# Kernel tuning notes

Measured on AMD Instinct MI355X. Metric: run time of the kernel, lower is better.

The kernel has to match this reference:

```python
import jax, jax.numpy as jnp
import numpy as np
from jax import lax

N_WIRES = 4
EPS_BN = 1e-5

def _conv(x, w, b):
    y = lax.conv_general_dilated(x, w, (1, 1), 'SAME',
                                 dimension_numbers=('NCHW', 'OIHW', 'NCHW'))
    return y + b[None, :, None, None]

def _bn2d(x, g, b):
    mu = jnp.mean(x, axis=(0, 2, 3), keepdims=True)
    var = jnp.var(x, axis=(0, 2, 3), keepdims=True)
    return (x - mu) * lax.rsqrt(var + EPS_BN) * g[None, :, None, None] + b[None, :, None, None]

def _maxpool2(x):
    return lax.reduce_window(x, -jnp.inf, lax.max, (1, 1, 2, 2), (1, 1, 2, 2), 'VALID')

def _ry(t):
    c, s = jnp.cos(t / 2), jnp.sin(t / 2)
    return jnp.stack([jnp.stack([c, -s], -1), jnp.stack([s, c], -1)], -2).astype(jnp.complex64)

def _rz(t):
    tc = t.astype(jnp.complex64)
    em, ep = jnp.exp(-0.5j * tc), jnp.exp(0.5j * tc)
    z = jnp.zeros_like(em)
    return jnp.stack([jnpp_stack := jnp.stack([em, z], -1), jnp.stack([z, ep], -1)], -2)

def _rx(t):
    c = jnp.cos(t / 2).astype(jnp.complex64)
    s = (-1j) * jnp.sin(t / 2).astype(jnp.complex64)
    return jnp.stack([jnp.stack([c, s], -1), jnp.stack([s, c], -1)], -2)

def _apply_1q(state, U, q):
    # state: (B,2,2,2,2); U: (2,2) shared or (B,2,2) per-sample
    a = jnp.moveaxis(state, 1 + q, 1)
    if U.ndim == 2:
        a = jnp.einsum('ij,bj...->bi...', U, a)
    else:
        a = jnp.einsum('bij,bj...->bi...', U, a)
    return jnp.moveaxis(a, 1, 1 + q)

def _cnot(state, c, t):
    a = jnp.moveaxis(state, (1 + c, 1 + t), (1, 2))
    a = jnp.stack([a[:, 0], jnp.flip(a[:, 1], axis=1)], axis=1)
    return jnp.moveaxis(a, (1, 2), (1 + c, 1 + t))

def _circuit(scaled, theta, rho):
    # scaled: (B, 4) angles; theta, rho: (4, 3)
    B = scaled.shape[0]
    state = jnp.zeros((B,) + (2,) * N_WIRES, jnp.complex64)
    state = state.at[(slice(None),) + (0,) * N_WIRES].set(1.0 + 0j)
    for i in range(N_WIRES):
        state = _apply_1q(state, _ry(scaled[:, i]), i)
    for i in range(N_WIRES):
        state = _apply_1q(state, _ry(theta[i, 0]), i)
        state = _apply_1q(state, _rz(theta[i, 1]), i)
        state = _apply_1q(state, _rx(theta[i, 2]), i)
    for i in range(N_WIRES - 1):
        state = _cnot(state, i, i + 1)
    for i in range(N_WIRES):
        state = _apply_1q(state, _ry(rho[i, 0]), i)
        state = _apply_1q(state, _rz(rho[i, 1]), i)
        state = _apply_1q(state, _rx(rho[i, 2]), i)
    for i in range(N_WIRES - 1):
        state = _cnot(state, i + 1, i)
    probs = jnp.abs(state) ** 2  # (B,2,2,2,2)
    exps = []
    for i in range(N_WIRES):
        p = jnp.moveaxis(probs, 1 + i, 1)
        exps.append(jnp.sum(p[:, 0], axis=(1, 2, 3)) - jnp.sum(p[:, 1], axis=(1, 2, 3)))
    return jnp.stack(exps, axis=1)  # (B,4)

def setup_inputs() -> dict:
    key = jax.random.key(0)
    ks = jax.random.split(key, 8)
    B = 128
    return {
        'x': jax.random.normal(ks[0], (B, 1, 224, 224), jnp.float32),
        'conv1_w': jax.random.normal(ks[1], (8, 1, 3, 3), jnp.float32) * 0.1,
        'conv1_b': jnp.zeros((8,), jnp.float32),
        'bn1_g': jnp.ones((8,), jnp.float32),
        'bn1_b': jnp.zeros((8,), jnp.float32),
        'conv2_w': jax.random.normal(ks[2], (16, 8, 3, 3), jnp.float32) * 0.1,
        'conv2_b': jnp.zeros((16,), jnp.float32),
        'bn2_g': jnp.ones((16,), jnp.float32),
        'bn2_b': jnp.zeros((16,), jnp.float32),
        'theta': jax.random.normal(ks[3], (4, 3), jnp.float32),
        'rho': jax.random.normal(ks[4], (4, 3), jnp.float32),
        'norm_g': jnp.ones((4,), jnp.float32),
        'norm_b': jnp.zeros((4,), jnp.float32),
    }

def reference(x, conv1_w, conv1_b, bn1_g, bn1_b, conv2_w, conv2_b, bn2_g, bn2_b,
              theta, rho, norm_g, norm_b):
    h = jax.nn.relu(_bn2d(_conv(x, conv1_w, conv1_b), bn1_g, bn1_b))
    h = _maxpool2(h)
    h = jax.nn.relu(_bn2d(_conv(h, conv2_w, conv2_b), bn2_g, bn2_b))
    h = _maxpool2(h)
    feat = jnp.mean(h, axis=(2, 3))          # AdaptiveAvgPool2d((1,1)) + flatten -> (B,16)
    feat = feat[:, :N_WIRES]                  # (B,4)
    scaled = (feat - jnp.mean(feat)) / (jnp.std(feat, ddof=1) + 1e-6) * jnp.pi
    out = _circuit(scaled, theta, rho)        # (B,4) real
    mu = jnp.mean(out, axis=0, keepdims=True)
    var = jnp.var(out, axis=0, keepdims=True)
    return (out - mu) * lax.rsqrt(var + EPS_BN) * norm_g[None, :] + norm_b[None, :]
```

## Files before the change

### kernel.cpp

```cpp
#include <hip/hip_runtime.h>
#include <math.h>

#define H1 224
#define W1 224
#define H2 112
#define W2 112
#define HP 56
#define WP 56

#define NS 32
#define SLOT_STRIDE 64

struct C2 { float re, im; };
__device__ __forceinline__ C2 cmul(C2 a, C2 b) {
    return C2{fmaf(a.re, b.re, -a.im * b.im), fmaf(a.re, b.im, a.im * b.re)};
}
__device__ __forceinline__ C2 cadd(C2 a, C2 b) { return C2{a.re + b.re, a.im + b.im}; }

template <int S>
__device__ __forceinline__ void ap1s(C2* st, C2 u00, C2 u01, C2 u10, C2 u11) {
#pragma unroll
    for (int i = 0; i < 16; i++) {
        if (i & S) continue;
        C2 a0 = st[i], a1 = st[i + S];
        st[i]     = cadd(cmul(u00, a0), cmul(u01, a1));
        st[i + S] = cadd(cmul(u10, a0), cmul(u11, a1));
    }
}
template <int SC, int STT>
__device__ __forceinline__ void cnot_s(C2* st) {
#pragma unroll
    for (int i = 0; i < 16; i++)
        if ((i & SC) && !(i & STT)) { C2 t = st[i]; st[i] = st[i + STT]; st[i + STT] = t; }
}
struct M2 { C2 m[2][2]; };
__device__ __forceinline__ M2 mmul(const M2& A, const M2& B) {
    M2 R;
#pragma unroll
    for (int i = 0; i < 2; i++)
#pragma unroll
        for (int j = 0; j < 2; j++)
            R.m[i][j] = cadd(cmul(A.m[i][0], B.m[0][j]), cmul(A.m[i][1], B.m[1][j]));
    return R;
}
__device__ __forceinline__ M2 combined_u(const float* __restrict__ p) {
    float c0 = cosf(0.5f * p[0]), s0 = sinf(0.5f * p[0]);
    float c1 = cosf(0.5f * p[1]), s1 = sinf(0.5f * p[1]);
    float c2 = cosf(0.5f * p[2]), s2 = sinf(0.5f * p[2]);
    M2 Ry = {{{{c0, 0.f}, {-s0, 0.f}}, {{s0, 0.f}, {c0, 0.f}}}};
    M2 Rz = {{{{c1, -s1}, {0.f, 0.f}}, {{0.f, 0.f}, {c1, s1}}}};
    M2 Rx = {{{{c2, 0.f}, {0.f, -s2}}, {{0.f, -s2}, {c2, 0.f}}}};
    return mmul(Rx, mmul(Rz, Ry));
}

template <int Q>
__device__ __forceinline__ void rows_reduce(float* red, const float* vals, int tid) {
#pragma unroll
    for (int q = 0; q < Q; q++) red[q * 256 + tid] = vals[q];
    __syncthreads();
#pragma unroll
    for (int s = 128; s > 0; s >>= 1) {
        for (int idx = tid; idx < Q * s; idx += 256) {
            int row = idx / s, i = idx - row * s;
            red[row * 256 + i] += red[row * 256 + i + s];
        }
        __syncthreads();
    }
}

__global__ void zero_ws(float* ws, int n) {
    int i = blockIdx.x * blockDim.x + threadIdx.x;
    if (i < n) ws[i] = 0.f;
}

__device__ __forceinline__ float slot_sum(const float* stats, int c) {
    float s = 0.f;
#pragma unroll
    for (int sl = 0; sl < NS; sl++) s += stats[sl * SLOT_STRIDE + c];
    return s;
}

__global__ void conv1_pool_stats(const float* __restrict__ x, const float* __restrict__ w,
                                 const float* __restrict__ bias, const float* __restrict__ g1,
                                 float* __restrict__ stats, float* __restrict__ p1ext) {
    __shared__ float red[16 * 256];
    int strip = blockIdx.x;
    int b = blockIdx.y;
    int tid = threadIdx.x;
    const float* xb = x + (size_t)b * H1 * W1;
    float sums[8], sqs[8], pm[8], ext8[8];
    bool gp[8];
#pragma unroll
    for (int c = 0; c < 8; c++) { sums[c] = 0.f; sqs[c] = 0.f; gp[c] = g1[c] >= 0.f; }
    int col = tid;
    if (col < W1) {
        bool cl = col > 0, cr = col < W1 - 1;
        int row0 = strip * 8;
        float a0, a1, a2, b0, b1, b2, c0, c1, c2;
        {
            int r = row0 - 1;
            if (r >= 0) {
                a0 = cl ? xb[r * W1 + col - 1] : 0.f;
                a1 = xb[r * W1 + col];
                a2 = cr ? xb[r * W1 + col + 1] : 0.f;
            } else { a0 = a1 = a2 = 0.f; }
            r = row0;
            b0 = cl ? xb[r * W1 + col - 1] : 0.f;
            b1 = xb[r * W1 + col];
            b2 = cr ? xb[r * W1 + col + 1] : 0.f;
        }
        for (int rr = 0; rr < 8; rr++) {
            int rn = row0 + rr + 1;
            if (rn < H1) {
                c0 = cl ? xb[rn * W1 + col - 1] : 0.f;
                c1 = xb[rn * W1 + col];
                c2 = cr ? xb[rn * W1 + col + 1] : 0.f;
            } else { c0 = c1 = c2 = 0.f; }
#pragma unroll
            for (int c = 0; c < 8; c++) {
                float acc = bias[c];
                acc = fmaf(w[c * 9 + 0], a0, acc);
                acc = fmaf(w[c * 9 + 1], a1, acc);
                acc = fmaf(w[c * 9 + 2], a2, acc);
                acc = fmaf(w[c * 9 + 3], b0, acc);
                acc = fmaf(w[c * 9 + 4], b1, acc);
                acc = fmaf(w[c * 9 + 5], b2, acc);
                acc = fmaf(w[c * 9 + 6], c0, acc);
                acc = fmaf(w[c * 9 + 7], c1, acc);
                acc = fmaf(w[c * 9 + 8], c2, acc);
                sums[c] += acc;
                sqs[c] = fmaf(acc, acc, sqs[c]);
                if ((rr & 1) == 0) {
                    pm[c] = acc;
                } else {
                    float m = gp[c] ? fmaxf(pm[c], acc) : fminf(pm[c], acc);
                    float mo = __shfl_xor(m, 1, 64);
                    ext8[c] = gp[c] ? fmaxf(m, mo) : fminf(m, mo);
                }
            }
            if ((rr & 1) == 1 && (col & 1) == 0) {
                int prow = strip * 4 + (rr >> 1);
                int pcol = col >> 1;
                float* dst = p1ext + ((((size_t)b * H2 + prow) * W2 + pcol) << 3);
                ((float4*)dst)[0] = make_float4(ext8[0], ext8[1], ext8[2], ext8[3]);
                ((float4*)dst)[1] = make_float4(ext8[4], ext8[5], ext8[6], ext8[7]);
            }
            a0 = b0; a1 = b1; a2 = b2;
            b0 = c0; b1 = c1; b2 = c2;
        }
    }
    float vals[16];
#pragma unroll
    for (int c = 0; c < 8; c++) { vals[c] = sums[c]; vals[8 + c] = sqs[c]; }
    rows_reduce<16>(red, vals, tid);
    int slot = (b * 28 + strip) & (NS - 1);
    if (tid < 16) atomicAdd(stats + slot * SLOT_STRIDE + tid, red[tid * 256]);
}

__global__ void conv1_stats(const float* __restrict__ x, const float* __restrict__ w,
                            const float* __restrict__ bias, float* __restrict__ stats) {
    __shared__ float red[16 * 256];
    int strip = blockIdx.x;
    int b = blockIdx.y;
    int tid = threadIdx.x;
    const float* xb = x + (size_t)b * H1 * W1;
    float sums[8], sqs[8];
#pragma unroll
    for (int c = 0; c < 8; c++) { sums[c] = 0.f; sqs[c] = 0.f; }
    int col = tid;
    if (col < W1) {
        bool cl = col > 0, cr = col < W1 - 1;
        int row0 = strip * 8;
        float a0, a1, a2, b0, b1, b2, c0, c1, c2;
        {
            int r = row0 - 1;
            if (r >= 0) {
                a0 = cl ? xb[r * W1 + col - 1] : 0.f;
                a1 = xb[r * W1 + col];
                a2 = cr ? xb[r * W1 + col + 1] : 0.f;
            } else { a0 = a1 = a2 = 0.f; }
            r = row0;
            b0 = cl ? xb[r * W1 + col - 1] : 0.f;
            b1 = xb[r * W1 + col];
            b2 = cr ? xb[r * W1 + col + 1] : 0.f;
        }
        for (int rr = 0; rr < 8; rr++) {
            int rn = row0 + rr + 1;
            if (rn < H1) {
                c0 = cl ? xb[rn * W1 + col - 1] : 0.f;
                c1 = xb[rn * W1 + col];
                c2 = cr ? xb[rn * W1 + col + 1] : 0.f;
            } else { c0 = c1 = c2 = 0.f; }
#pragma unroll
            for (int c = 0; c < 8; c++) {
                float acc = bias[c];
                acc = fmaf(w[c * 9 + 0], a0, acc);
                acc = fmaf(w[c * 9 + 1], a1, acc);
                acc = fmaf(w[c * 9 + 2], a2, acc);
                acc = fmaf(w[c * 9 + 3], b0, acc);
                acc = fmaf(w[c * 9 + 4], b1, acc);
                acc = fmaf(w[c * 9 + 5], b2, acc);
                acc = fmaf(w[c * 9 + 6], c0, acc);
                acc = fmaf(w[c * 9 + 7], c1, acc);
                acc = fmaf(w[c * 9 + 8], c2, acc);
                sums[c] += acc;
                sqs[c] = fmaf(acc, acc, sqs[c]);
            }
            a0 = b0; a1 = b1; a2 = b2;
            b0 = c0; b1 = c1; b2 = c2;
        }
    }
    float vals[16];
#pragma unroll
    for (int c = 0; c < 8; c++) { vals[c] = sums[c]; vals[8 + c] = sqs[c]; }
    rows_reduce<16>(red, vals, tid);
    int slot = (b * 28 + strip) & (NS - 1);
    if (tid < 16) atomicAdd(stats + slot * SLOT_STRIDE + tid, red[tid * 256]);
}

template <int PH, int PW>
__device__ __forceinline__ void build_h1_tile(const float* __restrict__ xb,
                                              float (*h1t)[PH][PW],
                                              const float* __restrict__ w1,
                                              const float* __restrict__ b1,
                                              const float* sc1, const float* sh1,
                                              int oy0, int ox0, int tid) {
    for (int i = tid; i < PH * PW; i += 256) {
        int p = i / PW, q = i % PW;
        int hy = oy0 + p, hx = ox0 + q;
        bool ok = (hy >= 0 && hy < H2 && hx >= 0 && hx < W2);
        float xp[5][5];
        if (hy >= 1 && hy <= H2 - 2 && hx >= 1 && hx <= W2 - 2) {
            const float* bp = xb + (2 * hy - 1) * W1 + (2 * hx - 1);
#pragma unroll
            for (int r = 0; r < 5; r++)
#pragma unroll
                for (int c = 0; c < 5; c++) xp[r][c] = bp[r * W1 + c];
        } else if (ok) {
#pragma unroll
            for (int r = 0; r < 5; r++)
#pragma unroll
                for (int c = 0; c < 5; c++) {
                    int gy = 2 * hy - 1 + r, gx = 2 * hx - 1 + c;
                    xp[r][c] = (gy >= 0 && gy < H1 && gx >= 0 && gx < W1) ? xb[gy * W1 + gx] : 0.f;
                }
        }
#pragma unroll
        for (int c = 0; c < 8; c++) {
            float mx = 0.f;
            if (ok) {
                mx = -INFINITY;
#pragma unroll
                for (int dy = 0; dy < 2; dy++)
#pragma unroll
                    for (int dx = 0; dx < 2; dx++) {
                        float acc = b1[c];
#pragma unroll
                        for (int ky = 0; ky < 3; ky++)
#pragma unroll
                            for (int kx = 0; kx < 3; kx++)
                                acc = fmaf(w1[c * 9 + ky * 3 + kx], xp[dy + ky][dx + kx], acc);
                        mx = fmaxf(mx, fmaxf(fmaf(acc, sc1[c], sh1[c]), 0.f));
                    }
            }
            h1t[c][p][q] = mx;
        }
    }
}

__global__ __launch_bounds__(256, 4) void conv2_stats_slim(
        const float* __restrict__ p1ext, const float* __restrict__ g1,
        const float* __restrict__ be1, const float* __restrict__ stats1,
        const float* __restrict__ w2, const float* __restrict__ b2,
        const float* __restrict__ g2,
        float* __restrict__ stats2, float* __restrict__ p2ext, float N1) {
    __shared__ __align__(16) float h1t[8][34][34];
    __shared__ float sc1[8], sh1[8];
    int b = blockIdx.z;
    int Y0 = blockIdx.y * 32, X0 = blockIdx.x * 32;
    int ty = threadIdx.y, tx = threadIdx.x;
    int tid = ty * 16 + tx;
    if (tid < 8) {
        float su = slot_sum(stats1, tid), sq = slot_sum(stats1, 8 + tid);
        float mu = su / N1;
        float var = sq / N1 - mu * mu;
        float sc = g1[tid] * rsqrtf(var + 1e-5f);
        sc1[tid] = sc;
        sh1[tid] = be1[tid] - mu * sc;
    }
    __syncthreads();
    const float* pb = p1ext + (((size_t)b * H2) * W2 << 3);
    for (int i = tid; i < 34 * 34; i += 256) {
        int p = i / 34, q = i % 34;
        int hy = Y0 - 1 + p, hx = X0 - 1 + q;
        if (hy >= 0 && hy < H2 && hx >= 0 && hx < W2) {
            const float* cp = pb + (((size_t)hy * W2 + hx) << 3);
            float4 u = ((const float4*)cp)[0];
            float4 v = ((const float4*)cp)[1];
            h1t[0][p][q] = fmaxf(fmaf(u.x, sc1[0], sh1[0]), 0.f);
            h1t[1][p][q] = fmaxf(fmaf(u.y, sc1[1], sh1[1]), 0.f);
            h1t[2][p][q] = fmaxf(fmaf(u.z, sc1[2], sh1[2]), 0.f);
            h1t[3][p][q] = fmaxf(fmaf(u.w, sc1[3], sh1[3]), 0.f);
            h1t[4][p][q] = fmaxf(fmaf(v.x, sc1[4], sh1[4]), 0.f);
            h1t[5][p][q] = fmaxf(fmaf(v.y, sc1[5], sh1[5]), 0.f);
            h1t[6][p][q] = fmaxf(fmaf(v.z, sc1[6], sh1[6]), 0.f);
            h1t[7][p][q] = fmaxf(fmaf(v.w, sc1[7], sh1[7]), 0.f);
        } else {
#pragma unroll
            for (int c = 0; c < 8; c++) h1t[c][p][q] = 0.f;
        }
    }
    __syncthreads();
    float acc[4][2][2];
#pragma unroll
    for (int co = 0; co < 4; co++)
#pragma unroll
        for (int dy = 0; dy < 2; dy++)
#pragma unroll
            for (int dx = 0; dx < 2; dx++) acc[co][dy][dx] = b2[co];
#pragma unroll
    for (int ci = 0; ci < 8; ci++) {
        float win[4][4];
#pragma unroll
        for (int r = 0; r < 4; r++) {
            const float2* rp = (const float2*)&h1t[ci][2 * ty + r][2 * tx];
            float2 u = rp[0], v = rp[1];
            win[r][0] = u.x; win[r][1] = u.y; win[r][2] = v.x; win[r][3] = v.y;
        }
#pragma unroll
        for (int co = 0; co < 4; co++)
#pragma unroll
            for (int ky = 0; ky < 3; ky++)
#pragma unroll
                for (int kx = 0; kx < 3; kx++) {
                    float wv = w2[co * 72 + ci * 9 + ky * 3 + kx];
#pragma unroll
                    for (int dy = 0; dy < 2; dy++)
#pragma unroll
                        for (int dx = 0; dx < 2; dx++)
                            acc[co][dy][dx] = fmaf(wv, win[dy + ky][dx + kx], acc[co][dy][dx]);
                }
    }
    int cy0 = Y0 + 2 * ty, cx0 = X0 + 2 * tx;
    bool vy0 = cy0 < H2, vy1 = cy0 + 1 < H2, vx0 = cx0 < W2, vx1 = cx0 + 1 < W2;
    float vals[8];
#pragma unroll
    for (int co = 0; co < 4; co++) {
        float s = 0.f, q = 0.f;
        if (vy0 && vx0) { float a = acc[co][0][0]; s += a; q = fmaf(a, a, q); }
        if (vy0 && vx1) { float a = acc[co][0][1]; s += a; q = fmaf(a, a, q); }
        if (vy1 && vx0) { float a = acc[co][1][0]; s += a; q = fmaf(a, a, q); }
        if (vy1 && vx1) { float a = acc[co][1][1]; s += a; q = fmaf(a, a, q); }
        vals[co] = s;
        vals[4 + co] = q;
    }
    {
        int hy = (Y0 >> 1) + ty, hx = (X0 >> 1) + tx;
        if (hy < HP && hx < WP) {
#pragma unroll
            for (int co = 0; co < 4; co++) {
                float mx = fmaxf(fmaxf(acc[co][0][0], acc[co][0][1]),
                                 fmaxf(acc[co][1][0], acc[co][1][1]));
                float mn = fminf(fminf(acc[co][0][0], acc[co][0][1]),
                                 fminf(acc[co][1][0], acc[co][1][1]));
                p2ext[(((size_t)b * 4 + co) * HP + hy) * WP + hx] = (g2[co] >= 0.f) ? mx : mn;
            }
        }
    }
    __syncthreads();
    float* red = (float*)h1t;
    rows_reduce<8>(red, vals, tid);
    int slot = ((b * 16) + blockIdx.y * 4 + blockIdx.x) & (NS - 1);
    if (tid < 8) atomicAdd(stats2 + slot * SLOT_STRIDE + tid, red[tid * 256]);
}

template <bool STORE>
__global__ __launch_bounds__(256, 4) void conv2_stats_fused(
        const float* __restrict__ x, const float* __restrict__ w1,
        const float* __restrict__ b1, const float* __restrict__ g1,
        const float* __restrict__ be1, const float* __restrict__ stats1,
        const float* __restrict__ w2, const float* __restrict__ b2,
        float* __restrict__ stats2,
        float* __restrict__ pmax, float* __restrict__ pmin, float N1) {
    __shared__ __align__(16) float h1t[8][34][34];
    __shared__ float sc1[8], sh1[8];
    int b = blockIdx.z;
    int Y0 = blockIdx.y * 32, X0 = blockIdx.x * 32;
    int ty = threadIdx.y, tx = threadIdx.x;
    int tid = ty * 16 + tx;
    if (tid < 8) {
        float su = slot_sum(stats1, tid), sq = slot_sum(stats1, 8 + tid);
        float mu = su / N1;
        float var = sq / N1 - mu * mu;
        float sc = g1[tid] * rsqrtf(var + 1e-5f);
        sc1[tid] = sc;
        sh1[tid] = be1[tid] - mu * sc;
    }
    __syncthreads();
    const float* xb = x + (size_t)b * H1 * W1;
    build_h1_tile<34, 34>(xb, h1t, w1, b1, sc1, sh1, Y0 - 1, X0 - 1, tid);
    __syncthreads();
    float acc[4][2][2];
#pragma unroll
    for (int co = 0; co < 4; co++)
#pragma unroll
        for (int dy = 0; dy < 2; dy++)
#pragma unroll
            for (int dx = 0; dx < 2; dx++) acc[co][dy][dx] = b2[co];
#pragma unroll
    for (int ci = 0; ci < 8; ci++) {
        float win[4][4];
#pragma unroll
        for (int r = 0; r < 4; r++) {
            const float2* rp = (const float2*)&h1t[ci][2 * ty + r][2 * tx];
            float2 u = rp[0], v = rp[1];
            win[r][0] = u.x; win[r][1] = u.y; win[r][2] = v.x; win[r][3] = v.y;
        }
#pragma unroll
        for (int co = 0; co < 4; co++)
#pragma unroll
            for (int ky = 0; ky < 3; ky++)
#pragma unroll
                for (int kx = 0; kx < 3; kx++) {
                    float wv = w2[co * 72 + ci * 9 + ky * 3 + kx];
#pragma unroll
                    for (int dy = 0; dy < 2; dy++)
#pragma unroll
                        for (int dx = 0; dx < 2; dx++)
                            acc[co][dy][dx] = fmaf(wv, win[dy + ky][dx + kx], acc[co][dy][dx]);
                }
    }
    int cy0 = Y0 + 2 * ty, cx0 = X0 + 2 * tx;
    bool vy0 = cy0 < H2, vy1 = cy0 + 1 < H2, vx0 = cx0 < W2, vx1 = cx0 + 1 < W2;
    float vals[8];
#pragma unroll
    for (int co = 0; co < 4; co++) {
        float s = 0.f, q = 0.f;
        if (vy0 && vx0) { float a = acc[co][0][0]; s += a; q = fmaf(a, a, q); }
        if (vy0 && vx1) { float a = acc[co][0][1]; s += a; q = fmaf(a, a, q); }
        if (vy1 && vx0) { float a = acc[co][1][0]; s += a; q = fmaf(a, a, q); }
        if (vy1 && vx1) { float a = acc[co][1][1]; s += a; q = fmaf(a, a, q); }
        vals[co] = s;
        vals[4 + co] = q;
    }
    if (STORE) {
        int hy = (Y0 >> 1) + ty, hx = (X0 >> 1) + tx;
        if (hy < HP && hx < WP) {
#pragma unroll
            for (int co = 0; co < 4; co++) {
                float mx = fmaxf(fmaxf(acc[co][0][0], acc[co][0][1]),
                                 fmaxf(acc[co][1][0], acc[co][1][1]));
                float mn = fminf(fminf(acc[co][0][0], acc[co][0][1]),
                                 fminf(acc[co][1][0], acc[co][1][1]));
                size_t idx = (((size_t)b * 4 + co) * HP + hy) * WP + hx;
                pmax[idx] = mx;
                pmin[idx] = mn;
            }
        }
    }
    __syncthreads();
    float* red = (float*)h1t;
    rows_reduce<8>(red, vals, tid);
    int slot = ((b * 16) + blockIdx.y * 4 + blockIdx.x) & (NS - 1);
    if (tid < 8) atomicAdd(stats2 + slot * SLOT_STRIDE + tid, red[tid * 256]);
}

__global__ void pool_bn_mean(const float* __restrict__ pmax, const float* __restrict__ pmin,
                             const float* __restrict__ g2, const float* __restrict__ be2,
                             const float* __restrict__ stats2,
                             float* __restrict__ featbuf, float N2) {
    __shared__ float red[256];
    int co = blockIdx.x & 3;
    int b = blockIdx.x >> 2;
    int tid = threadIdx.x;
    float su = slot_sum(stats2, co), sq = slot_sum(stats2, 4 + co);
    float mu = su / N2;
    float var = sq / N2 - mu * mu;
    float sc = g2[co] * rsqrtf(var + 1e-5f);
    float sh = be2[co] - mu * sc;
    const float* P = (sc >= 0.f ? pmax : pmin) + ((size_t)b * 4 + co) * (HP * WP);
    float s = 0.f;
    for (int i = tid; i < HP * WP; i += 256) s += fmaxf(fmaf(P[i], sc, sh), 0.f);
    red[tid] = s;
    __syncthreads();
    for (int st = 128; st > 0; st >>= 1) {
        if (tid < st) red[tid] += red[tid + st];
        __syncthreads();
    }
    if (tid == 0) featbuf[(size_t)b * 4 + co] = red[0];
}

__global__ void conv2_final_fused(const float* __restrict__ x, const float* __restrict__ w1,
                                  const float* __restrict__ b1, const float* __restrict__ g1,
                                  const float* __restrict__ be1,
                                  const float* __restrict__ stats1,
                                  const float* __restrict__ w2, const float* __restrict__ b2,
                                  const float* __restrict__ g2, const float* __restrict__ be2,
                                  const float* __restrict__ stats2,
                                  float* __restrict__ featbuf, float N1, float N2) {
    __shared__ __align__(16) float h1t[8][34][34];
    __shared__ float sc1[8], sh1[8];
    __shared__ float sc2[4], sh2[4];
    int b = blockIdx.z;
    int py0 = blockIdx.y * 16, px0 = blockIdx.x * 16;
    int ty = threadIdx.y, tx = threadIdx.x;
    int tid = ty * 16 + tx;
    if (tid < 8) {
        float su = slot_sum(stats1, tid), sq = slot_sum(stats1, 8 + tid);
        float mu = su / N1;
        float var = sq / N1 - mu * mu;
        float sc = g1[tid] * rsqrtf(var + 1e-5f);
        sc1[tid] = sc;
        sh1[tid] = be1[tid] - mu * sc;
    }
    if (tid >= 16 && tid < 20) {
        int j = tid - 16;
        float su = slot_sum(stats2, j), sq = slot_sum(stats2, 4 + j);
        float mu = su / N2;
        float var = sq / N2 - mu * mu;
        float sc = g2[j] * rsqrtf(var + 1e-5f);
        sc2[j] = sc;
        sh2[j] = be2[j] - mu * sc;
    }
    __syncthreads();
    const float* xb = x + (size_t)b * H1 * W1;
    build_h1_tile<34, 34>(xb, h1t, w1, b1, sc1, sh1, 2 * py0 - 1, 2 * px0 - 1, tid);
    __syncthreads();
    bool valid = (py0 + ty < HP) && (px0 + tx < WP);
    float acc[4][2][2];
#pragma unroll
    for (int co = 0; co < 4; co++)
#pragma unroll
        for (int dy = 0; dy < 2; dy++)
#pragma unroll
            for (int dx = 0; dx < 2; dx++) acc[co][dy][dx] = b2[co];
#pragma unroll
    for (int ci = 0; ci < 8; ci++) {
        float win[4][4];
#pragma unroll
        for (int r = 0; r < 4; r++) {
            const float2* rp = (const float2*)&h1t[ci][2 * ty + r][2 * tx];
            float2 u = rp[0], v = rp[1];
            win[r][0] = u.x; win[r][1] = u.y; win[r][2] = v.x; win[r][3] = v.y;
        }
#pragma unroll
        for (int co = 0; co < 4; co++)
#pragma unroll
            for (int ky = 0; ky < 3; ky++)
#pragma unroll
                for (int kx = 0; kx < 3; kx++) {
                    float wv = w2[co * 72 + ci * 9 + ky * 3 + kx];
#pragma unroll
                    for (int dy = 0; dy < 2; dy++)
#pragma unroll
                        for (int dx = 0; dx < 2; dx++)
                            acc[co][dy][dx] = fmaf(wv, win[dy + ky][dx + kx], acc[co][dy][dx]);
                }
    }
    float vals[4];
#pragma unroll
    for (int co = 0; co < 4; co++) {
        float mx = -INFINITY;
#pragma unroll
        for (int dy = 0; dy < 2; dy++)
#pragma unroll
            for (int dx = 0; dx < 2; dx++)
                mx = fmaxf(mx, fmaxf(fmaf(acc[co][dy][dx], sc2[co], sh2[co]), 0.f));
        vals[co] = valid ? mx : 0.f;
    }
    __syncthreads();
    float* red = (float*)h1t;
    rows_reduce<4>(red, vals, tid);
    if (tid < 4) atomicAdd(featbuf + (size_t)b * 4 + tid, red[tid * 256]);
}

__device__ __forceinline__ float bsum(float v, float* lds) {
#pragma unroll
    for (int off = 32; off; off >>= 1) v += __shfl_xor(v, off, 64);
    __syncthreads();
    if ((threadIdx.x & 63) == 0) lds[threadIdx.x >> 6] = v;
    __syncthreads();
    float r = 0.f;
    int nw = (int)(blockDim.x + 63) >> 6;
#pragma clang loop unroll(disable)
    for (int i = 0; i < nw; i++) r += lds[i];
    return r;
}

__global__ void finalize(const float* __restrict__ featbuf, const float* __restrict__ theta,
                         const float* __restrict__ rho, const float* __restrict__ ng,
                         const float* __restrict__ nb, float* __restrict__ out, int B) {
    __shared__ float lds[16];
    int b = threadIdx.x;
    float f[4];
#pragma unroll
    for (int j = 0; j < 4; j++) f[j] = featbuf[b * 4 + j] * (1.f / (HP * WP));
    float n = 4.f * (float)B;
    float mean = bsum(f[0] + f[1] + f[2] + f[3], lds) / n;
    float d2 = 0.f;
#pragma unroll
    for (int j = 0; j < 4; j++) { float d = f[j] - mean; d2 += d * d; }
    float var1 = bsum(d2, lds) / (n - 1.f);
    float stdv = sqrtf(fmaxf(var1, 0.f)) + 1e-6f;
    const float PI = 3.14159265358979323846f;
    float cs[4], sn[4];
#pragma unroll
    for (int j = 0; j < 4; j++) {
        float sc = (f[j] - mean) / stdv * PI;
        cs[j] = cosf(0.5f * sc);
        sn[j] = sinf(0.5f * sc);
    }
    C2 st[16];
    {
        float amp[16];
        amp[1] = sn[3]; amp[0] = cs[3];
#pragma unroll
        for (int k = 0; k < 2; k++) { amp[k + 2] = amp[k] * sn[2]; amp[k] *= cs[2]; }
#pragma unroll
        for (int k = 0; k < 4; k++) { amp[k + 4] = amp[k] * sn[1]; amp[k] *= cs[1]; }
#pragma unroll
        for (int k = 0; k < 8; k++) { amp[k + 8] = amp[k] * sn[0]; amp[k] *= cs[0]; }
#pragma unroll
        for (int i = 0; i < 16; i++) st[i] = C2{amp[i], 0.f};
    }
#pragma clang loop unroll(disable)
    for (int l = 0; l < 2; l++) {
        const float* p = (l == 0) ? theta : rho;
#pragma clang loop unroll(disable)
        for (int i = 0; i < 4; i++) {
            M2 U = combined_u(p + i * 3);
            switch (i) {
            case 0: ap1s<8>(st, U.m[0][0], U.m[0][1], U.m[1][0], U.m[1][1]); break;
            case 1: ap1s<4>(st, U.m[0][0], U.m[0][1], U.m[1][0], U.m[1][1]); break;
            case 2: ap1s<2>(st, U.m[0][0], U.m[0][1], U.m[1][0], U.m[1][1]); break;
            default: ap1s<1>(st, U.m[0][0], U.m[0][1], U.m[1][0], U.m[1][1]); break;
            }
        }
        if (l == 0) { cnot_s<8, 4>(st); cnot_s<4, 2>(st); cnot_s<2, 1>(st); }
        else        { cnot_s<4, 8>(st); cnot_s<2, 4>(st); cnot_s<1, 2>(st); }
    }
    float e[4];
#pragma unroll
    for (int qb = 0; qb < 4; qb++) {
        int m = 8 >> qb;
        float p0 = 0.f, p1 = 0.f;
#pragma unroll
        for (int i = 0; i < 16; i++) {
            float pr = st[i].re * st[i].re + st[i].im * st[i].im;
            if (i & m) p1 += pr; else p0 += pr;
        }
        e[qb] = p0 - p1;
    }
#pragma clang loop unroll(disable)
    for (int j = 0; j < 4; j++) {
        float mu = bsum(e[j], lds) / (float)B;
        float dv = e[j] - mu;
        float v = bsum(dv * dv, lds) / (float)B;
        out[b * 4 + j] = fmaf(dv, rsqrtf(v + 1e-5f) * ng[j], nb[j]);
    }
}

extern "C" void kernel_launch(void* const* d_in, const int* in_sizes, int n_in,
                              void* d_out, int out_size, void* d_ws, size_t ws_size,
                              hipStream_t stream) {
    const float* x     = (const float*)d_in[0];
    const float* w1    = (const float*)d_in[1];
    const float* b1    = (const float*)d_in[2];
    const float* g1    = (const float*)d_in[3];
    const float* be1   = (const float*)d_in[4];
    const float* w2    = (const float*)d_in[5];
    const float* b2    = (const float*)d_in[6];
    const float* g2    = (const float*)d_in[7];
    const float* be2   = (const float*)d_in[8];
    const float* theta = (const float*)d_in[9];
    const float* rho   = (const float*)d_in[10];
    const float* ng    = (const float*)d_in[11];
    const float* nb    = (const float*)d_in[12];
    float* out = (float*)d_out;

    int B = in_sizes[0] / (H1 * W1);

    float* ws = (float*)d_ws;
    float* stats1 = ws;
    float* stats2 = ws + NS * SLOT_STRIDE;
    float* featbuf = ws + 2 * NS * SLOT_STRIDE;
    float* bufs = featbuf + (size_t)B * 4;

    size_t common = (size_t)(2 * NS * SLOT_STRIDE) + (size_t)B * 4;
    size_t p2n = (size_t)B * 4 * HP * WP;
    size_t p1n = (size_t)B * 8 * H2 * W2;
    size_t needA = (common + p2n + p1n) * sizeof(float);
    size_t needB = (common + 2 * p2n) * sizeof(float);
    bool tierA = ws_size >= needA;
    bool tierB = !tierA && ws_size >= needB;

    float N1 = (float)B * H1 * W1;
    float N2 = (float)B * H2 * W2;
    int nz = (int)common;

    zero_ws<<<(nz + 255) / 256, 256, 0, stream>>>(ws, nz);
    if (tierA) {
        float* p2ext = bufs;
        float* p1ext = bufs + p2n;
        conv1_pool_stats<<<dim3(28, B), 256, 0, stream>>>(x, w1, b1, g1, stats1, p1ext);
        conv2_stats_slim<<<dim3(4, 4, B), dim3(16, 16), 0, stream>>>(
            p1ext, g1, be1, stats1, w2, b2, g2, stats2, p2ext, N1);
        pool_bn_mean<<<B * 4, 256, 0, stream>>>(p2ext, p2ext, g2, be2, stats2, featbuf, N2);
        finalize<<<1, B, 0, stream>>>(featbuf, theta, rho, ng, nb, out, B);
    } else if (tierB) {
        float* pmax = bufs;
        float* pmin = bufs + p2n;
        conv1_stats<<<dim3(28, B), 256, 0, stream>>>(x, w1, b1, stats1);
        conv2_stats_fused<true><<<dim3(4, 4, B), dim3(16, 16), 0, stream>>>(
            x, w1, b1, g1, be1, stats1, w2, b2, stats2, pmax, pmin, N1);
        pool_bn_mean<<<B * 4, 256, 0, stream>>>(pmax, pmin, g2, be2, stats2, featbuf, N2);
        finalize<<<1, B, 0, stream>>>(featbuf, theta, rho, ng, nb, out, B);
    } else {
        conv1_stats<<<dim3(28, B), 256, 0, stream>>>(x, w1, b1, stats1);
        conv2_stats_fused<false><<<dim3(4, 4, B), dim3(16, 16), 0, stream>>>(
            x, w1, b1, g1, be1, stats1, w2, b2, stats2, nullptr, nullptr, N1);
        conv2_final_fused<<<dim3(4, 4, B), dim3(16, 16), 0, stream>>>(
            x, w1, b1, g1, be1, stats1, w2, b2, g2, be2, stats2, featbuf, N1, N2);
        finalize<<<1, B, 0, stream>>>(featbuf, theta, rho, ng, nb, out, B);
    }
}
```

Baseline: 176.9 us.

## Compute two adjacent conv1 columns per thread to pool without shuffles

Each thread of conv1_pool_stats now handles two horizontally adjacent output pixels (one pooled column), with the two 128-thread halves of the block covering different 8-row bands. The grid drops from 28 to 14 strips per image. Both outputs reuse one float2 load plus the two edge values, and the horizontal pool becomes a local max/min, which removes the cross-lane shuffle and the idle odd lanes during stores. A launch-bounds hint is added and the row loop is fully unrolled. The cost is higher register pressure and fewer blocks in the grid.

```diff
diff --git a/kernel.cpp b/kernel.cpp
--- a/kernel.cpp
+++ b/kernel.cpp
@@ -80,80 +80,85 @@
     return s;
 }
 
-__global__ void conv1_pool_stats(const float* __restrict__ x, const float* __restrict__ w,
-                                 const float* __restrict__ bias, const float* __restrict__ g1,
-                                 float* __restrict__ stats, float* __restrict__ p1ext) {
+__global__ __launch_bounds__(256, 2) void conv1_pool_stats(
+        const float* __restrict__ x, const float* __restrict__ w,
+        const float* __restrict__ bias, const float* __restrict__ g1,
+        float* __restrict__ stats, float* __restrict__ p1ext) {
     __shared__ float red[16 * 256];
     int strip = blockIdx.x;
     int b = blockIdx.y;
     int tid = threadIdx.x;
+    int pc = tid & 127;
+    int rhalf = tid >> 7;
+    int r0 = strip * 16 + rhalf * 8;
     const float* xb = x + (size_t)b * H1 * W1;
-    float sums[8], sqs[8], pm[8], ext8[8];
+    float sums[8], sqs[8], pm[8];
     bool gp[8];
 #pragma unroll
     for (int c = 0; c < 8; c++) { sums[c] = 0.f; sqs[c] = 0.f; gp[c] = g1[c] >= 0.f; }
-    int col = tid;
-    if (col < W1) {
-        bool cl = col > 0, cr = col < W1 - 1;
-        int row0 = strip * 8;
-        float a0, a1, a2, b0, b1, b2, c0, c1, c2;
+    bool act = pc < W2;
+    if (act) {
+        bool cl = pc > 0, cr = pc < W2 - 1;
+        const float* rp0 = xb + (size_t)r0 * W1 + 2 * pc;
+        float al, am0, am1, ar, bl, bm0, bm1, br;
+        if (r0 > 0) {
+            const float* rp = rp0 - W1;
+            float2 m = *(const float2*)rp;
+            al = cl ? rp[-1] : 0.f; am0 = m.x; am1 = m.y; ar = cr ? rp[2] : 0.f;
+        } else { al = 0.f; am0 = 0.f; am1 = 0.f; ar = 0.f; }
         {
-            int r = row0 - 1;
-            if (r >= 0) {
-                a0 = cl ? xb[r * W1 + col - 1] : 0.f;
-                a1 = xb[r * W1 + col];
-                a2 = cr ? xb[r * W1 + col + 1] : 0.f;
-            } else { a0 = a1 = a2 = 0.f; }
-            r = row0;
-            b0 = cl ? xb[r * W1 + col - 1] : 0.f;
-            b1 = xb[r * W1 + col];
-            b2 = cr ? xb[r * W1 + col + 1] : 0.f;
-        }
+            float2 m = *(const float2*)rp0;
+            bl = cl ? rp0[-1] : 0.f; bm0 = m.x; bm1 = m.y; br = cr ? rp0[2] : 0.f;
+        }
+#pragma unroll
         for (int rr = 0; rr < 8; rr++) {
-            int rn = row0 + rr + 1;
+            float nl = 0.f, nm0 = 0.f, nm1 = 0.f, nr = 0.f;
+            int rn = r0 + rr + 1;
             if (rn < H1) {
-                c0 = cl ? xb[rn * W1 + col - 1] : 0.f;
-                c1 = xb[rn * W1 + col];
-                c2 = cr ? xb[rn * W1 + col + 1] : 0.f;
-            } else { c0 = c1 = c2 = 0.f; }
+                const float* rp = rp0 + (size_t)(rr + 1) * W1;
+                float2 m = *(const float2*)rp;
+                nl = cl ? rp[-1] : 0.f; nm0 = m.x; nm1 = m.y; nr = cr ? rp[2] : 0.f;
+            }
+            float4 e0 = make_float4(0.f, 0.f, 0.f, 0.f);
+            float4 e1 = make_float4(0.f, 0.f, 0.f, 0.f);
 #pragma unroll
             for (int c = 0; c < 8; c++) {
-                float acc = bias[c];
-                acc = fmaf(w[c * 9 + 0], a0, acc);
-                acc = fmaf(w[c * 9 + 1], a1, acc);
-                acc = fmaf(w[c * 9 + 2], a2, acc);
-                acc = fmaf(w[c * 9 + 3], b0, acc);
-                acc = fmaf(w[c * 9 + 4], b1, acc);
-                acc = fmaf(w[c * 9 + 5], b2, acc);
-                acc = fmaf(w[c * 9 + 6], c0, acc);
-                acc = fmaf(w[c * 9 + 7], c1, acc);
-                acc = fmaf(w[c * 9 + 8], c2, acc);
-                sums[c] += acc;
-                sqs[c] = fmaf(acc, acc, sqs[c]);
+                const float* wc = w + c * 9;
+                float y0 = bias[c], y1 = bias[c];
+                y0 = fmaf(wc[0], al,  y0); y0 = fmaf(wc[1], am0, y0); y0 = fmaf(wc[2], am1, y0);
+                y1 = fmaf(wc[0], am0, y1); y1 = fmaf(wc[1], am1, y1); y1 = fmaf(wc[2], ar,  y1);
+                y0 = fmaf(wc[3], bl,  y0); y0 = fmaf(wc[4], bm0, y0); y0 = fmaf(wc[5], bm1, y0);
+                y1 = fmaf(wc[3], bm0, y1); y1 = fmaf(wc[4], bm1, y1); y1 = fmaf(wc[5], br,  y1);
+                y0 = fmaf(wc[6], nl,  y0); y0 = fmaf(wc[7], nm0, y0); y0 = fmaf(wc[8], nm1, y0);
+                y1 = fmaf(wc[6], nm0, y1); y1 = fmaf(wc[7], nm1, y1); y1 = fmaf(wc[8], nr,  y1);
+                sums[c] += y0 + y1;
+                sqs[c] = fmaf(y0, y0, fmaf(y1, y1, sqs[c]));
+                float m01 = gp[c] ? fmaxf(y0, y1) : fminf(y0, y1);
                 if ((rr & 1) == 0) {
-                    pm[c] = acc;
+                    pm[c] = m01;
                 } else {
-                    float m = gp[c] ? fmaxf(pm[c], acc) : fminf(pm[c], acc);
-                    float mo = __shfl_xor(m, 1, 64);
-                    ext8[c] = gp[c] ? fmaxf(m, mo) : fminf(m, mo);
+                    float e = gp[c] ? fmaxf(pm[c], m01) : fminf(pm[c], m01);
+                    if (c == 0) e0.x = e; else if (c == 1) e0.y = e;
+                    else if (c == 2) e0.z = e; else if (c == 3) e0.w = e;
+                    else if (c == 4) e1.x = e; else if (c == 5) e1.y = e;
+                    else if (c == 6) e1.z = e; else e1.w = e;
                 }
             }
-            if ((rr & 1) == 1 && (col & 1) == 0) {
-                int prow = strip * 4 + (rr >> 1);
-                int pcol = col >> 1;
-                float* dst = p1ext + ((((size_t)b * H2 + prow) * W2 + pcol) << 3);
-                ((float4*)dst)[0] = make_float4(ext8[0], ext8[1], ext8[2], ext8[3]);
-                ((float4*)dst)[1] = make_float4(ext8[4], ext8[5], ext8[6], ext8[7]);
+            if (rr & 1) {
+                int pr = (r0 + rr) >> 1;
+                float* dst = p1ext + ((((size_t)b * H2 + pr) * W2 + pc) << 3);
+                ((float4*)dst)[0] = e0;
+                ((float4*)dst)[1] = e1;
             }
-            a0 = b0; a1 = b1; a2 = b2;
-            b0 = c0; b1 = c1; b2 = c2;
+            al = bl; am0 = bm0; am1 = bm1; ar = br;
+            bl = nl; bm0 = nm0; bm1 = nm1; br = nr;
         }
     }
     float vals[16];
 #pragma unroll
     for (int c = 0; c < 8; c++) { vals[c] = sums[c]; vals[8 + c] = sqs[c]; }
     rows_reduce<16>(red, vals, tid);
-    int slot = (b * 28 + strip) & (NS - 1);
+    int slot = (b * 14 + strip) & (NS - 1);
     if (tid < 16) atomicAdd(stats + slot * SLOT_STRIDE + tid, red[tid * 256]);
 }
 
@@ -702,7 +707,7 @@
     if (tierA) {
         float* p2ext = bufs;
         float* p1ext = bufs + p2n;
-        conv1_pool_stats<<<dim3(28, B), 256, 0, stream>>>(x, w1, b1, g1, stats1, p1ext);
+        conv1_pool_stats<<<dim3(14, B), 256, 0, stream>>>(x, w1, b1, g1, stats1, p1ext);
         conv2_stats_slim<<<dim3(4, 4, B), dim3(16, 16), 0, stream>>>(
             p1ext, g1, be1, stats1, w2, b2, g2, stats2, p2ext, N1);
         pool_bn_mean<<<B * 4, 256, 0, stream>>>(p2ext, p2ext, g2, be2, stats2, featbuf, N2);
```

After: 170.3 us. 3.7% less time.
